# Performance work log

Measured on AMD Instinct MI355X. Metric: run time of the kernel, lower is better.

## Reference

```python
import jax, jax.numpy as jnp
from jax import lax
import numpy as np

B, T, E, D, U = 64, 2048, 512, 1024, 128


def setup_inputs() -> dict:
    key = jax.random.key(0)
    ks = jax.random.split(key, 12)
    s = 0.05
    queries = jax.random.normal(ks[0], (B, 1, D), jnp.float32)
    prev = jax.random.uniform(ks[1], (B, T), jnp.float32)
    prev = prev / prev.sum(-1, keepdims=True)  # alignment-like (sums to 1)
    enc = jax.random.normal(ks[2], (B, T, E), jnp.float32)
    lengths = jax.random.randint(ks[3], (B,), 1, T + 1)
    conv_w = jax.random.normal(ks[4], (U, 1, 3), jnp.float32) * s   # (out,in,k)
    conv_b = jax.random.normal(ks[5], (U,), jnp.float32) * s
    Wq = jax.random.normal(ks[6], (U, D), jnp.float32) * s          # query_layer weight
    Wk = jax.random.normal(ks[7], (U, E), jnp.float32) * s          # key_layer weight
    v_w = jax.random.normal(ks[8], (1, U), jnp.float32) * s         # v weight
    v_b = jax.random.normal(ks[9], (1,), jnp.float32) * s           # v bias
    b = jax.random.uniform(ks[10], (U,), jnp.float32)               # nn.Parameter(torch.rand)
    return dict(queries=queries, previous_alignments=prev, encoder_output=enc,
                conv_w=conv_w, conv_b=conv_b, Wq=Wq, Wk=Wk, v_w=v_w, v_b=v_b,
                b=b, lengths=lengths)


def reference(queries, previous_alignments, encoder_output, conv_w, conv_b,
              Wq, Wk, v_w, v_b, b, lengths):
    Bt, Tt, Et = encoder_output.shape
    # set_memory: proj_key and mask
    proj_key = jnp.einsum('bte,ue->btu', encoder_output, Wk)          # (B,T,U)
    mask = jnp.arange(Tt)[None, :] >= lengths[:, None]                # (B,T)
    # conv1d on previous alignments, kernel 3, padding 1
    conv = lax.conv_general_dilated(previous_alignments[:, None, :], conv_w,
                                    window_strides=(1,), padding=[(1, 1)],
                                    dimension_numbers=('NCH', 'OIH', 'NCH'))
    conv_attn = (conv + conv_b[None, :, None]).transpose(0, 2, 1)     # (B,T,U)
    q_proj = jnp.einsum('bqd,ud->bqu', queries, Wq)                   # (B,1,U)
    w = jnp.tanh(q_proj + proj_key + conv_attn + b)                   # (B,T,U)
    score = jnp.einsum('btu,u->bt', w, v_w[0]) + v_b[0]               # (B,T)
    score = jnp.where(mask, -jnp.inf, score)
    attn_weight = jax.nn.softmax(score, axis=-1)                      # (B,T)
    context = jnp.einsum('bt,bte->be', attn_weight, encoder_output)[:, None, :]  # (B,1,E)
    return context, attn_weight
```

## Files before the change

### kernel.cpp

```cpp
#include <hip/hip_runtime.h>
#include <hip/hip_bf16.h>

typedef __bf16 bf16x8 __attribute__((ext_vector_type(8)));
typedef float  f32x4  __attribute__((ext_vector_type(4)));

#define Bsz 64
#define Tdim 2048
#define Edim 512
#define Ddim 1024
#define Udim 128
#define CHUNK 128
#define NCHUNK 16

__device__ inline bf16x8 cvt8(float4 a, float4 b) {
    bf16x8 h;
    h[0] = (__bf16)a.x; h[1] = (__bf16)a.y; h[2] = (__bf16)a.z; h[3] = (__bf16)a.w;
    h[4] = (__bf16)b.x; h[5] = (__bf16)b.y; h[6] = (__bf16)b.z; h[7] = (__bf16)b.w;
    return h;
}

__device__ inline float fast_tanh(float x) {
    float e = __expf(2.f * x);
    return 1.f - __fdividef(2.f, e + 1.f);
}

__global__ __launch_bounds__(256) void k_prep(const float* __restrict__ q,
                                              const float* __restrict__ Wq,
                                              const float* __restrict__ bparam,
                                              const float* __restrict__ convb,
                                              const float* __restrict__ Wk,
                                              unsigned short* __restrict__ wkbf,
                                              float* __restrict__ qb) {
    int bid = blockIdx.x, tid = threadIdx.x;
    if (bid >= 256) {
        int cb = bid - 256;
        #pragma unroll
        for (int k = 0; k < 2; ++k) {
            int E = (cb * 256 + tid) * 2 + k;
            int c8 = E & 7;
            int u  = (E >> 3) & 127;
            int es = E >> 10;
            const float* src = Wk + (size_t)u * Edim + es * 64 + c8 * 8;
            float4 a = *reinterpret_cast<const float4*>(src);
            float4 b = *reinterpret_cast<const float4*>(src + 4);
            int dst = es * 16384 + ((u * 128 + c8 * 16) ^ ((u & 7) << 4));
            *reinterpret_cast<bf16x8*>(reinterpret_cast<char*>(wkbf) + dst) = cvt8(a, b);
        }
        return;
    }
    int wg   = bid * 4 + (tid >> 6);
    int lane = tid & 63;
    int b  = wg >> 4;
    int u0 = (wg & 15) * 8;
    const float* qr = q + (size_t)b * Ddim + lane * 16;
    float4 qv[4];
    #pragma unroll
    for (int i = 0; i < 4; ++i) qv[i] = *reinterpret_cast<const float4*>(qr + i * 4);
    float s[8];
    #pragma unroll
    for (int jj = 0; jj < 8; ++jj) {
        const float* wr = Wq + (size_t)(u0 + jj) * Ddim + lane * 16;
        float acc = 0.f;
        #pragma unroll
        for (int i = 0; i < 4; ++i) {
            float4 w = *reinterpret_cast<const float4*>(wr + i * 4);
            acc += qv[i].x * w.x + qv[i].y * w.y + qv[i].z * w.z + qv[i].w * w.w;
        }
        s[jj] = acc;
    }
    #pragma unroll
    for (int m = 32; m; m >>= 1) {
        #pragma unroll
        for (int jj = 0; jj < 8; ++jj) s[jj] += __shfl_xor(s[jj], m);
    }
    if (lane == 0) {
        #pragma unroll
        for (int jj = 0; jj < 8; ++jj)
            qb[b * 128 + u0 + jj] = s[jj] + bparam[u0 + jj] + convb[u0 + jj];
    }
}

__global__ __launch_bounds__(256) void k_score_ctx(const float* __restrict__ enc,
                                                   const float* __restrict__ prev,
                                                   const unsigned short* __restrict__ wkbf,
                                                   const float* __restrict__ qb,
                                                   const float* __restrict__ conv_w,
                                                   const float* __restrict__ v_w,
                                                   const float* __restrict__ v_b,
                                                   const int* __restrict__ lengths,
                                                   float* __restrict__ score_out,
                                                   float* __restrict__ m_ws,
                                                   float* __restrict__ l_ws,
                                                   float* __restrict__ c_ws) {
    __shared__ alignas(16) unsigned short At[128 * 64];
    __shared__ alignas(16) unsigned short Bt[128 * 64];
    __shared__ float s_prev[130];
    __shared__ float s_qb[128];
    __shared__ float s_vw[128];
    __shared__ float s_cw[3][128];
    __shared__ float s_score[128];
    __shared__ float s_p[128];
    __shared__ alignas(16) float s_cred[128 * 4];

    const int tid   = threadIdx.x;
    const int b     = blockIdx.y;
    const int chunk = blockIdx.x;
    const int t0    = chunk * CHUNK;
    const int lane  = tid & 63, wid = tid >> 6;
    const int len   = lengths[b];
    const int pidx  = b * NCHUNK + chunk;

    if (t0 >= len) {
        if (tid == 0) { m_ws[pidx] = -3.4e38f; l_ws[pidx] = 0.f; }
        return;
    }

    if (tid < 128) {
        s_qb[tid]    = qb[b * 128 + tid];
        s_vw[tid]    = v_w[tid];
        s_cw[0][tid] = conv_w[tid * 3 + 0];
        s_cw[1][tid] = conv_w[tid * 3 + 1];
        s_cw[2][tid] = conv_w[tid * 3 + 2];
    }
    if (tid < 130) {
        int idx = t0 - 1 + tid;
        s_prev[tid] = (idx >= 0 && idx < Tdim) ? prev[b * Tdim + idx] : 0.f;
    }

    const float* encb = enc + ((size_t)b * Tdim + t0) * Edim;

    f32x4 acc[2][8];
    #pragma unroll
    for (int m2 = 0; m2 < 2; ++m2)
        #pragma unroll
        for (int n = 0; n < 8; ++n) acc[m2][n] = (f32x4){0.f, 0.f, 0.f, 0.f};

    for (int es = 0; es < 8; ++es) {
        const int e0 = es * 64;
        {
            const char* wsrc = reinterpret_cast<const char*>(wkbf) + es * 16384 + tid * 16;
            char* bdst = reinterpret_cast<char*>(Bt) + tid * 16;
            #pragma unroll
            for (int i = 0; i < 4; ++i) {
                __builtin_amdgcn_global_load_lds(
                    (const __attribute__((address_space(1))) unsigned int*)(wsrc + i * 4096),
                    (__attribute__((address_space(3))) unsigned int*)(bdst + i * 4096),
                    16, 0, 0);
            }
        }
        #pragma unroll
        for (int i = 0; i < 4; ++i) {
            int lin = tid + i * 256;
            int r = lin >> 3, c8 = lin & 7;
            const float* src = encb + (size_t)r * Edim + e0 + c8 * 8;
            float4 va  = *reinterpret_cast<const float4*>(src);
            float4 vb2 = *reinterpret_cast<const float4*>(src + 4);
            int off = (r * 128 + c8 * 16) ^ ((r & 7) << 4);
            *reinterpret_cast<bf16x8*>(reinterpret_cast<char*>(At) + off) = cvt8(va, vb2);
        }
        __syncthreads();
        #pragma unroll
        for (int kk = 0; kk < 2; ++kk) {
            bf16x8 af[2];
            #pragma unroll
            for (int m2 = 0; m2 < 2; ++m2) {
                int ar = wid * 32 + m2 * 16 + (lane & 15);
                int abyte = (ar * 128 + kk * 64 + (lane >> 4) * 16) ^ ((ar & 7) << 4);
                af[m2] = *reinterpret_cast<const bf16x8*>(reinterpret_cast<const char*>(At) + abyte);
            }
            #pragma unroll
            for (int n = 0; n < 8; ++n) {
                int br = n * 16 + (lane & 15);
                int bbyte = (br * 128 + kk * 64 + (lane >> 4) * 16) ^ ((br & 7) << 4);
                bf16x8 bv = *reinterpret_cast<const bf16x8*>(reinterpret_cast<const char*>(Bt) + bbyte);
                acc[0][n] = __builtin_amdgcn_mfma_f32_16x16x32_bf16(af[0], bv, acc[0][n], 0, 0, 0);
                acc[1][n] = __builtin_amdgcn_mfma_f32_16x16x32_bf16(af[1], bv, acc[1][n], 0, 0, 0);
            }
        }
        __syncthreads();
    }

    float sc[2][4] = {{0.f,0.f,0.f,0.f},{0.f,0.f,0.f,0.f}};
    #pragma unroll
    for (int m2 = 0; m2 < 2; ++m2) {
        #pragma unroll
        for (int n = 0; n < 8; ++n) {
            int u = n * 16 + (lane & 15);
            float c0 = s_cw[0][u], c1 = s_cw[1][u], c2 = s_cw[2][u];
            float qbu = s_qb[u], vwu = s_vw[u];
            #pragma unroll
            for (int j = 0; j < 4; ++j) {
                int tl = wid * 32 + m2 * 16 + (lane >> 4) * 4 + j;
                float conv = s_prev[tl] * c0 + s_prev[tl + 1] * c1 + s_prev[tl + 2] * c2;
                sc[m2][j] += vwu * fast_tanh(acc[m2][n][j] + qbu + conv);
            }
        }
    }
    #pragma unroll
    for (int m2 = 0; m2 < 2; ++m2)
        #pragma unroll
        for (int j = 0; j < 4; ++j) {
            sc[m2][j] += __shfl_xor(sc[m2][j], 1);
            sc[m2][j] += __shfl_xor(sc[m2][j], 2);
            sc[m2][j] += __shfl_xor(sc[m2][j], 4);
            sc[m2][j] += __shfl_xor(sc[m2][j], 8);
        }
    if ((lane & 15) == 0) {
        float vb = v_b[0];
        #pragma unroll
        for (int m2 = 0; m2 < 2; ++m2) {
            int tl = wid * 32 + m2 * 16 + (lane >> 4) * 4;
            #pragma unroll
            for (int j = 0; j < 4; ++j) {
                float s = sc[m2][j] + vb;
                s_score[tl + j] = s;
                score_out[b * Tdim + t0 + tl + j] = s;
            }
        }
    }
    __syncthreads();

    float sv0 = (t0 + lane < len)      ? s_score[lane]      : -3.4e38f;
    float sv1 = (t0 + 64 + lane < len) ? s_score[lane + 64] : -3.4e38f;
    float m = fmaxf(sv0, sv1);
    #pragma unroll
    for (int s = 32; s; s >>= 1) m = fmaxf(m, __shfl_xor(m, s));
    float p0 = (t0 + lane < len)      ? __expf(sv0 - m) : 0.f;
    float p1 = (t0 + 64 + lane < len) ? __expf(sv1 - m) : 0.f;
    float l = p0 + p1;
    #pragma unroll
    for (int s = 32; s; s >>= 1) l += __shfl_xor(l, s);
    if (tid < 64) { s_p[tid] = p0; s_p[tid + 64] = p1; }
    if (tid == 0) { m_ws[pidx] = m; l_ws[pidx] = l; }
    __syncthreads();

    {
        int e4 = (tid & 127) * 4;
        int th = tid >> 7;
        float4 a = make_float4(0.f, 0.f, 0.f, 0.f);
        #pragma unroll 4
        for (int t = th; t < CHUNK; t += 2) {
            float pt = s_p[t];
            float4 v = *reinterpret_cast<const float4*>(encb + (size_t)t * Edim + e4);
            a.x += pt * v.x; a.y += pt * v.y; a.z += pt * v.z; a.w += pt * v.w;
        }
        if (th == 1) *reinterpret_cast<float4*>(&s_cred[(tid & 127) * 4]) = a;
        __syncthreads();
        if (th == 0) {
            float4 o = *reinterpret_cast<const float4*>(&s_cred[tid * 4]);
            a.x += o.x; a.y += o.y; a.z += o.z; a.w += o.w;
            *reinterpret_cast<float4*>(c_ws + (size_t)pidx * Edim + e4) = a;
        }
    }
}

__global__ __launch_bounds__(256) void k_combine(const float* __restrict__ m_ws,
                                                 const float* __restrict__ l_ws,
                                                 const float* __restrict__ c_ws,
                                                 const int* __restrict__ lengths,
                                                 float* __restrict__ ctx,
                                                 float* __restrict__ attn) {
    int b = blockIdx.x, tid = threadIdx.x;
    int lane = tid & 63, wid = tid >> 6;
    __shared__ float s_w[NCHUNK];
    __shared__ float sM, sinvL;

    if (wid == 0) {
        float mj = (lane < NCHUNK) ? m_ws[b * NCHUNK + lane] : -3.4e38f;
        float lj = (lane < NCHUNK) ? l_ws[b * NCHUNK + lane] : 0.f;
        float M = mj;
        #pragma unroll
        for (int s = 32; s; s >>= 1) M = fmaxf(M, __shfl_xor(M, s));
        float w = (lj > 0.f) ? __expf(mj - M) : 0.f;
        float L = lj * w;
        #pragma unroll
        for (int s = 32; s; s >>= 1) L += __shfl_xor(L, s);
        if (lane < NCHUNK) s_w[lane] = w;
        if (lane == 0) { sM = M; sinvL = 1.f / L; }
    }
    __syncthreads();
    float M = sM, invL = sinvL;

    {
        int e2 = tid * 2;
        float ax = 0.f, ay = 0.f;
        #pragma unroll
        for (int j = 0; j < NCHUNK; ++j) {
            float w = s_w[j];
            if (w != 0.f) {
                float2 v = *reinterpret_cast<const float2*>(c_ws + ((size_t)(b * NCHUNK + j)) * Edim + e2);
                ax += w * v.x; ay += w * v.y;
            }
        }
        float2 r = make_float2(ax * invL, ay * invL);
        *reinterpret_cast<float2*>(ctx + (size_t)b * Edim + e2) = r;
    }

    int len = lengths[b];
    #pragma unroll
    for (int i = 0; i < Tdim / 256; ++i) {
        int t = tid + i * 256;
        float s = attn[(size_t)b * Tdim + t];
        attn[(size_t)b * Tdim + t] = (t < len) ? __expf(s - M) * invL : 0.f;
    }
}

extern "C" void kernel_launch(void* const* d_in, const int* in_sizes, int n_in,
                              void* d_out, int out_size, void* d_ws, size_t ws_size,
                              hipStream_t stream) {
    const float* queries = (const float*)d_in[0];
    const float* prev    = (const float*)d_in[1];
    const float* enc     = (const float*)d_in[2];
    const float* conv_w  = (const float*)d_in[3];
    const float* conv_b  = (const float*)d_in[4];
    const float* Wq      = (const float*)d_in[5];
    const float* Wk      = (const float*)d_in[6];
    const float* v_w     = (const float*)d_in[7];
    const float* v_b     = (const float*)d_in[8];
    const float* bparam  = (const float*)d_in[9];
    const int*   lengths = (const int*)d_in[10];

    float* out  = (float*)d_out;
    float* ctx  = out;
    float* attn = out + Bsz * Edim;

    char* ws = (char*)d_ws;
    unsigned short* wkbf = (unsigned short*)ws;
    float* qb   = (float*)(ws + 131072);
    float* m_ws = (float*)(ws + 163840);
    float* l_ws = (float*)(ws + 172032);
    float* c_ws = (float*)(ws + 196608);

    k_prep<<<272, 256, 0, stream>>>(queries, Wq, bparam, conv_b, Wk, wkbf, qb);
    k_score_ctx<<<dim3(NCHUNK, Bsz), 256, 0, stream>>>(enc, prev, wkbf, qb, conv_w, v_w, v_b,
                                                       lengths, attn, m_ws, l_ws, c_ws);
    k_combine<<<Bsz, 256, 0, stream>>>(m_ws, l_ws, c_ws, lengths, ctx, attn);
}
```

Before: 81.73 us.

## Double chunk size to 256 rows with 512-thread blocks and swapped grid order

Each score/context block now handles 256 time steps with 8 waves instead of 128 with 4. This halves the number of Wk tile loads per batch and the partial-softmax workspace entries. The grid is transposed so consecutive blocks span batches rather than chunks, and the softmax max/sum reduction now goes across waves through shared memory. The enc loads are batched into register groups before the bf16 conversion to raise memory-level parallelism. The trade-off is more LDS per block and fewer blocks to spread over compute units. Blocks past the sequence length also skip work at a coarser granularity.

After: 77.46 us, median of 2. 1.06x faster.

```diff
diff --git a/kernel.cpp b/kernel.cpp
--- a/kernel.cpp
+++ b/kernel.cpp
@@ -9,8 +9,8 @@
 #define Edim 512
 #define Ddim 1024
 #define Udim 128
-#define CHUNK 128
-#define NCHUNK 16
+#define CHUNK 256
+#define NCHUNK 8
 
 __device__ inline bf16x8 cvt8(float4 a, float4 b) {
     bf16x8 h;
@@ -80,31 +80,32 @@
     }
 }
 
-__global__ __launch_bounds__(256) void k_score_ctx(const float* __restrict__ enc,
-                                                   const float* __restrict__ prev,
-                                                   const unsigned short* __restrict__ wkbf,
-                                                   const float* __restrict__ qb,
-                                                   const float* __restrict__ conv_w,
-                                                   const float* __restrict__ v_w,
-                                                   const float* __restrict__ v_b,
-                                                   const int* __restrict__ lengths,
-                                                   float* __restrict__ score_out,
-                                                   float* __restrict__ m_ws,
-                                                   float* __restrict__ l_ws,
-                                                   float* __restrict__ c_ws) {
-    __shared__ alignas(16) unsigned short At[128 * 64];
+__global__ __launch_bounds__(512, 4) void k_score_ctx(const float* __restrict__ enc,
+                                                      const float* __restrict__ prev,
+                                                      const unsigned short* __restrict__ wkbf,
+                                                      const float* __restrict__ qb,
+                                                      const float* __restrict__ conv_w,
+                                                      const float* __restrict__ v_w,
+                                                      const float* __restrict__ v_b,
+                                                      const int* __restrict__ lengths,
+                                                      float* __restrict__ score_out,
+                                                      float* __restrict__ m_ws,
+                                                      float* __restrict__ l_ws,
+                                                      float* __restrict__ c_ws) {
+    __shared__ alignas(16) unsigned short At[256 * 64];
     __shared__ alignas(16) unsigned short Bt[128 * 64];
-    __shared__ float s_prev[130];
+    __shared__ float s_prev[258];
     __shared__ float s_qb[128];
     __shared__ float s_vw[128];
     __shared__ float s_cw[3][128];
-    __shared__ float s_score[128];
-    __shared__ float s_p[128];
-    __shared__ alignas(16) float s_cred[128 * 4];
+    __shared__ float s_score[256];
+    __shared__ float s_p[256];
+    __shared__ float s_redm[4], s_redl[4];
+    __shared__ alignas(16) float s_cred[3][128][4];
 
     const int tid   = threadIdx.x;
-    const int b     = blockIdx.y;
-    const int chunk = blockIdx.x;
+    const int b     = blockIdx.x;
+    const int chunk = blockIdx.y;
     const int t0    = chunk * CHUNK;
     const int lane  = tid & 63, wid = tid >> 6;
     const int len   = lengths[b];
@@ -122,51 +123,62 @@
         s_cw[1][tid] = conv_w[tid * 3 + 1];
         s_cw[2][tid] = conv_w[tid * 3 + 2];
     }
-    if (tid < 130) {
-        int idx = t0 - 1 + tid;
-        s_prev[tid] = (idx >= 0 && idx < Tdim) ? prev[b * Tdim + idx] : 0.f;
+    if (tid >= 128 && tid < 128 + 258) {
+        int k = tid - 128;
+        int idx = t0 - 1 + k;
+        s_prev[k] = (idx >= 0 && idx < Tdim) ? prev[b * Tdim + idx] : 0.f;
     }
 
     const float* encb = enc + ((size_t)b * Tdim + t0) * Edim;
 
     f32x4 acc[2][8];
     #pragma unroll
-    for (int m2 = 0; m2 < 2; ++m2)
-        #pragma unroll
-        for (int n = 0; n < 8; ++n) acc[m2][n] = (f32x4){0.f, 0.f, 0.f, 0.f};
+    for (int m = 0; m < 2; ++m)
+        #pragma unroll
+        for (int n = 0; n < 8; ++n) acc[m][n] = (f32x4){0.f, 0.f, 0.f, 0.f};
 
     for (int es = 0; es < 8; ++es) {
         const int e0 = es * 64;
         {
             const char* wsrc = reinterpret_cast<const char*>(wkbf) + es * 16384 + tid * 16;
             char* bdst = reinterpret_cast<char*>(Bt) + tid * 16;
-            #pragma unroll
-            for (int i = 0; i < 4; ++i) {
-                __builtin_amdgcn_global_load_lds(
-                    (const __attribute__((address_space(1))) unsigned int*)(wsrc + i * 4096),
-                    (__attribute__((address_space(3))) unsigned int*)(bdst + i * 4096),
-                    16, 0, 0);
-            }
-        }
-        #pragma unroll
-        for (int i = 0; i < 4; ++i) {
-            int lin = tid + i * 256;
-            int r = lin >> 3, c8 = lin & 7;
-            const float* src = encb + (size_t)r * Edim + e0 + c8 * 8;
-            float4 va  = *reinterpret_cast<const float4*>(src);
-            float4 vb2 = *reinterpret_cast<const float4*>(src + 4);
-            int off = (r * 128 + c8 * 16) ^ ((r & 7) << 4);
-            *reinterpret_cast<bf16x8*>(reinterpret_cast<char*>(At) + off) = cvt8(va, vb2);
+            __builtin_amdgcn_global_load_lds(
+                (const __attribute__((address_space(1))) unsigned int*)(wsrc),
+                (__attribute__((address_space(3))) unsigned int*)(bdst), 16, 0, 0);
+            __builtin_amdgcn_global_load_lds(
+                (const __attribute__((address_space(1))) unsigned int*)(wsrc + 8192),
+                (__attribute__((address_space(3))) unsigned int*)(bdst + 8192), 16, 0, 0);
+        }
+        #pragma unroll
+        for (int pass = 0; pass < 2; ++pass) {
+            float4 ra[4];
+            int lin0 = tid + pass * 1024;
+            #pragma unroll
+            for (int sl = 0; sl < 2; ++sl) {
+                int lin = lin0 + sl * 512;
+                int r = lin >> 3, c8 = lin & 7;
+                const float* src = encb + (size_t)r * Edim + e0 + c8 * 8;
+                ra[2 * sl]     = *reinterpret_cast<const float4*>(src);
+                ra[2 * sl + 1] = *reinterpret_cast<const float4*>(src + 4);
+            }
+            #pragma unroll
+            for (int sl = 0; sl < 2; ++sl) {
+                int lin = lin0 + sl * 512;
+                int r = lin >> 3, c8 = lin & 7;
+                int off = (r * 128 + c8 * 16) ^ ((r & 7) << 4);
+                *reinterpret_cast<bf16x8*>(reinterpret_cast<char*>(At) + off) =
+                    cvt8(ra[2 * sl], ra[2 * sl + 1]);
+            }
         }
         __syncthreads();
         #pragma unroll
         for (int kk = 0; kk < 2; ++kk) {
             bf16x8 af[2];
             #pragma unroll
-            for (int m2 = 0; m2 < 2; ++m2) {
-                int ar = wid * 32 + m2 * 16 + (lane & 15);
+            for (int m = 0; m < 2; ++m) {
+                int ar = wid * 32 + m * 16 + (lane & 15);
                 int abyte = (ar * 128 + kk * 64 + (lane >> 4) * 16) ^ ((ar & 7) << 4);
-                af[m2] = *reinterpret_cast<const bf16x8*>(reinterpret_cast<const char*>(At) + abyte);
+                af[m] = *reinterpret_cast<const bf16x8*>(reinterpret_cast<const char*>(At) + abyte);
             }
             #pragma unroll
             for (int n = 0; n < 8; ++n) {
@@ -182,7 +194,7 @@
 
     float sc[2][4] = {{0.f,0.f,0.f,0.f},{0.f,0.f,0.f,0.f}};
     #pragma unroll
-    for (int m2 = 0; m2 < 2; ++m2) {
+    for (int m = 0; m < 2; ++m) {
         #pragma unroll
         for (int n = 0; n < 8; ++n) {
             int u = n * 16 + (lane & 15);
@@ -190,65 +202,81 @@
             float qbu = s_qb[u], vwu = s_vw[u];
             #pragma unroll
             for (int j = 0; j < 4; ++j) {
-                int tl = wid * 32 + m2 * 16 + (lane >> 4) * 4 + j;
-                float conv = s_prev[tl] * c0 + s_prev[tl + 1] * c1 + s_prev[tl + 2] * c2;
-                sc[m2][j] += vwu * fast_tanh(acc[m2][n][j] + qbu + conv);
-            }
-        }
-    }
-    #pragma unroll
-    for (int m2 = 0; m2 < 2; ++m2)
+                int r = wid * 32 + m * 16 + (lane >> 4) * 4 + j;
+                float conv = s_prev[r] * c0 + s_prev[r + 1] * c1 + s_prev[r + 2] * c2;
+                sc[m][j] += vwu * fast_tanh(acc[m][n][j] + qbu + conv);
+            }
+        }
+    }
+    #pragma unroll
+    for (int m = 0; m < 2; ++m)
         #pragma unroll
         for (int j = 0; j < 4; ++j) {
-            sc[m2][j] += __shfl_xor(sc[m2][j], 1);
-            sc[m2][j] += __shfl_xor(sc[m2][j], 2);
-            sc[m2][j] += __shfl_xor(sc[m2][j], 4);
-            sc[m2][j] += __shfl_xor(sc[m2][j], 8);
+            sc[m][j] += __shfl_xor(sc[m][j], 1);
+            sc[m][j] += __shfl_xor(sc[m][j], 2);
+            sc[m][j] += __shfl_xor(sc[m][j], 4);
+            sc[m][j] += __shfl_xor(sc[m][j], 8);
         }
     if ((lane & 15) == 0) {
         float vb = v_b[0];
         #pragma unroll
-        for (int m2 = 0; m2 < 2; ++m2) {
-            int tl = wid * 32 + m2 * 16 + (lane >> 4) * 4;
+        for (int m = 0; m < 2; ++m) {
+            int r = wid * 32 + m * 16 + (lane >> 4) * 4;
             #pragma unroll
             for (int j = 0; j < 4; ++j) {
-                float s = sc[m2][j] + vb;
-                s_score[tl + j] = s;
-                score_out[b * Tdim + t0 + tl + j] = s;
+                float s = sc[m][j] + vb;
+                s_score[r + j] = s;
+                score_out[b * Tdim + t0 + r + j] = s;
             }
         }
     }
     __syncthreads();
 
-    float sv0 = (t0 + lane < len)      ? s_score[lane]      : -3.4e38f;
-    float sv1 = (t0 + 64 + lane < len) ? s_score[lane + 64] : -3.4e38f;
-    float m = fmaxf(sv0, sv1);
-    #pragma unroll
-    for (int s = 32; s; s >>= 1) m = fmaxf(m, __shfl_xor(m, s));
-    float p0 = (t0 + lane < len)      ? __expf(sv0 - m) : 0.f;
-    float p1 = (t0 + 64 + lane < len) ? __expf(sv1 - m) : 0.f;
-    float l = p0 + p1;
-    #pragma unroll
-    for (int s = 32; s; s >>= 1) l += __shfl_xor(l, s);
-    if (tid < 64) { s_p[tid] = p0; s_p[tid + 64] = p1; }
-    if (tid == 0) { m_ws[pidx] = m; l_ws[pidx] = l; }
+    float sv = 0.f;
+    if (tid < 256) sv = (t0 + tid < len) ? s_score[tid] : -3.4e38f;
+    {
+        float m = (tid < 256) ? sv : -3.4e38f;
+        #pragma unroll
+        for (int s = 32; s; s >>= 1) m = fmaxf(m, __shfl_xor(m, s));
+        if (tid < 256 && lane == 0) s_redm[wid] = m;
+    }
     __syncthreads();
+    float M = fmaxf(fmaxf(s_redm[0], s_redm[1]), fmaxf(s_redm[2], s_redm[3]));
+    float p = 0.f;
+    if (tid < 256) {
+        p = (t0 + tid < len) ? __expf(sv - M) : 0.f;
+        s_p[tid] = p;
+    }
+    {
+        float l = (tid < 256) ? p : 0.f;
+        #pragma unroll
+        for (int s = 32; s; s >>= 1) l += __shfl_xor(l, s);
+        if (tid < 256 && lane == 0) s_redl[wid] = l;
+    }
+    __syncthreads();
+    if (tid == 0) {
+        m_ws[pidx] = M;
+        l_ws[pidx] = s_redl[0] + s_redl[1] + s_redl[2] + s_redl[3];
+    }
 
     {
         int e4 = (tid & 127) * 4;
-        int th = tid >> 7;
+        int tg = tid >> 7;
         float4 a = make_float4(0.f, 0.f, 0.f, 0.f);
         #pragma unroll 4
-        for (int t = th; t < CHUNK; t += 2) {
+        for (int t = tg; t < CHUNK; t += 4) {
             float pt = s_p[t];
             float4 v = *reinterpret_cast<const float4*>(encb + (size_t)t * Edim + e4);
             a.x += pt * v.x; a.y += pt * v.y; a.z += pt * v.z; a.w += pt * v.w;
         }
-        if (th == 1) *reinterpret_cast<float4*>(&s_cred[(tid & 127) * 4]) = a;
+        if (tg > 0) *reinterpret_cast<float4*>(&s_cred[tg - 1][tid & 127][0]) = a;
         __syncthreads();
-        if (th == 0) {
-            float4 o = *reinterpret_cast<const float4*>(&s_cred[tid * 4]);
-            a.x += o.x; a.y += o.y; a.z += o.z; a.w += o.w;
+        if (tg == 0) {
+            #pragma unroll
+            for (int g = 0; g < 3; ++g) {
+                float4 o = *reinterpret_cast<const float4*>(&s_cred[g][tid][0]);
+                a.x += o.x; a.y += o.y; a.z += o.z; a.w += o.w;
+            }
             *reinterpret_cast<float4*>(c_ws + (size_t)pidx * Edim + e4) = a;
         }
     }
@@ -292,8 +320,7 @@
                 ax += w * v.x; ay += w * v.y;
             }
         }
-        float2 r = make_float2(ax * invL, ay * invL);
-        *reinterpret_cast<float2*>(ctx + (size_t)b * Edim + e2) = r;
+        *reinterpret_cast<float2*>(ctx + (size_t)b * Edim + e2) = make_float2(ax * invL, ay * invL);
     }
 
     int len = lengths[b];
@@ -332,7 +359,7 @@
     float* c_ws = (float*)(ws + 196608);
 
     k_prep<<<272, 256, 0, stream>>>(queries, Wq, bparam, conv_b, Wk, wkbf, qb);
-    k_score_ctx<<<dim3(NCHUNK, Bsz), 256, 0, stream>>>(enc, prev, wkbf, qb, conv_w, v_w, v_b,
+    k_score_ctx<<<dim3(Bsz, NCHUNK), 512, 0, stream>>>(enc, prev, wkbf, qb, conv_w, v_w, v_b,
                                                        lengths, attn, m_ws, l_ws, c_ws);
     k_combine<<<Bsz, 256, 0, stream>>>(m_ws, l_ws, c_ws, lengths, ctx, attn);
 }
```
